# Kernel optimization log

Measured on AMD Instinct MI355X. Metric: run time of the kernel, lower is better.

Reference implementation:

```python
import jax, jax.numpy as jnp
import numpy as np

# raster settings (match init_kwargs)
H, W = 512, 512
TANFOVX, TANFOVY = 0.5, 0.5
DENSITY_SHIFT = -2.0
SCALE_MOD = 1.0
SH_DEG = 2
N, R, D = 262144, 8, 8

SH_C0 = 0.28209479177387814
SH_C1 = 0.4886025119029199
SH_C2 = (1.0925484305920792, -1.0925484305920792, 0.31539156525252005,
         -1.0925484305920792, 0.5462742152960396)


def _camera():
    # row-vector convention: p_view = p_world @ V[:3,:3] + V[3,:3]
    view = np.eye(4, dtype=np.float32)
    view[3, 2] = 3.0  # camera at (0,0,-3) looking down +z
    znear, zfar = 0.01, 100.0
    top, right = TANFOVY * znear, TANFOVX * znear
    P = np.zeros((4, 4), np.float32)
    P[0, 0] = znear / right
    P[1, 1] = znear / top
    P[2, 2] = zfar / (zfar - znear)
    P[2, 3] = 1.0
    P[3, 2] = -zfar * znear / (zfar - znear)
    proj = view @ P  # full world->clip, row-vector convention
    campos = np.array([0.0, 0.0, -3.0], np.float32)
    return jnp.asarray(view), jnp.asarray(proj), jnp.asarray(campos)


def setup_inputs() -> dict:
    key = jax.random.key(0)
    ks = jax.random.split(key, 6)
    positions = jax.random.uniform(ks[0], (N, 3), jnp.float32)          # local coords in [0,1]
    trivecs = jax.random.normal(ks[1], (N, R, 3, D), jnp.float32)
    densities = jax.random.normal(ks[2], (N, R), jnp.float32)
    shs = jax.random.normal(ks[3], (N, R, (SH_DEG + 1) ** 2, 3), jnp.float32) * 0.3
    view, proj, campos = _camera()
    aabb = jnp.array([-1.0, -1.0, -1.0, 2.0, 2.0, 2.0], jnp.float32)    # [origin, size]
    bg = jnp.zeros((3,), jnp.float32)
    rnd = jnp.full((H, W, 3), 0.5, jnp.float32)
    rnd = rnd.at[..., 2].set(jax.random.uniform(ks[4], (H, W), jnp.float32))
    return {"positions": positions, "trivecs": trivecs, "densities": densities,
            "shs": shs, "viewmatrix": view, "projmatrix": proj, "campos": campos,
            "aabb": aabb, "bg": bg, "random_image": rnd}


def _rasterize(positions, trivecs, densities, shs, viewmatrix, projmatrix, campos, aabb, bg):
    world = aabb[:3] + positions * aabb[3:]                              # [N,3]
    ones = jnp.ones((world.shape[0], 1), world.dtype)
    ph = jnp.concatenate([world, ones], 1) @ projmatrix                  # [N,4]
    ndc = ph[:, :3] / (ph[:, 3:4] + 1e-7)
    pview = world @ viewmatrix[:3, :3] + viewmatrix[3, :3]
    depth = pview[:, 2]                                                  # [N]
    ix = jnp.round(((ndc[:, 0] + 1.0) * W - 1.0) * 0.5).astype(jnp.int32)
    iy = jnp.round(((ndc[:, 1] + 1.0) * H - 1.0) * 0.5).astype(jnp.int32)
    valid = (depth > 0.2) & (ix >= 0) & (ix < W) & (iy >= 0) & (iy < H)
    pid = jnp.where(valid, iy * W + ix, H * W)                           # dump bucket H*W

    # trivec density at the cell center: product of the three axis vectors
    mid = trivecs[:, :, :, D // 2]                                       # [N,R,3]
    tri = jax.nn.relu(jnp.prod(mid, axis=-1))                            # [N,R]
    sigma_r = jnp.exp(densities + DENSITY_SHIFT) * tri * SCALE_MOD       # [N,R]
    sigma = sigma_r.sum(-1)
    alpha = jnp.clip(1.0 - jnp.exp(-sigma), 0.0, 0.999)                  # [N]

    # per-rank SH color, density-weighted over ranks
    dirs = world - campos
    dirs = dirs / (jnp.linalg.norm(dirs, axis=-1, keepdims=True) + 1e-8)
    x, y, z = dirs[:, 0:1], dirs[:, 1:2], dirs[:, 2:3]
    basis = jnp.concatenate([
        jnp.full_like(x, SH_C0),
        -SH_C1 * y, SH_C1 * z, -SH_C1 * x,
        SH_C2[0] * x * y, SH_C2[1] * y * z,
        SH_C2[2] * (2.0 * z * z - x * x - y * y),
        SH_C2[3] * x * z, SH_C2[4] * (x * x - y * y)], axis=1)           # [N,9]
    color_r = jnp.maximum(jnp.einsum('nk,nrkc->nrc', basis, shs) + 0.5, 0.0)
    wr = sigma_r / (sigma + 1e-8)[:, None]
    color = jnp.einsum('nr,nrc->nc', wr, color_r)                        # [N,3]

    # depth-sorted per-pixel alpha compositing via segmented exclusive cumsum
    order = jnp.lexsort((depth, pid))
    pid_s, a_s = pid[order], alpha[order]
    c_s, d_s = color[order], depth[order]
    logs = jnp.log1p(-a_s)
    excl = jnp.cumsum(logs) - logs                                       # exclusive cumsum
    first = jnp.searchsorted(pid_s, pid_s, side='left')                  # segment start idx
    T = jnp.exp(excl - excl[first])                                      # transmittance
    wgt = a_s * T
    npx = H * W
    img_c = jax.ops.segment_sum(wgt[:, None] * c_s, pid_s, num_segments=npx + 1)[:npx]
    img_a = jax.ops.segment_sum(wgt, pid_s, num_segments=npx + 1)[:npx]
    img_d = jax.ops.segment_sum(wgt * d_s, pid_s, num_segments=npx + 1)[:npx]
    img_c = img_c + (1.0 - img_a)[:, None] * bg
    pct_d = img_d / (img_a + 1e-8)
    return (img_c.reshape(H, W, 3).transpose(2, 0, 1),
            img_d.reshape(H, W), img_a.reshape(H, W), pct_d.reshape(H, W))


def reference(positions, trivecs, densities, shs, viewmatrix, projmatrix, campos, aabb, bg, random_image):
    # random_image is only used for stochastic jitter in the CUDA kernel; deterministic here
    return _rasterize(positions, trivecs, densities, shs, viewmatrix, projmatrix, campos, aabb, bg)
```

## Files before the change

kernel.cpp:

```cpp
#include <hip/hip_runtime.h>
#include <math.h>
#include <float.h>

#define Hh 512
#define Ww 512
#define HWW (Hh*Ww)
#define NP 262144
#define RR 8


__global__ __launch_bounds__(256) void point_kernel(
    const float* __restrict__ positions,
    const float* __restrict__ trivecs,
    const float* __restrict__ densities,
    const float* __restrict__ shs,
    const float* __restrict__ viewm,
    const float* __restrict__ projm,
    const float* __restrict__ campos,
    const float* __restrict__ aabb,
    float* __restrict__ recs,
    int* __restrict__ counts)
{
#pragma clang fp contract(off)
    int n = blockIdx.x * blockDim.x + threadIdx.x;
    if (n >= NP) return;

    float px = positions[n*3+0], py = positions[n*3+1], pz = positions[n*3+2];
    float wx = aabb[0] + px*aabb[3];
    float wy = aabb[1] + py*aabb[4];
    float wz = aabb[2] + pz*aabb[5];

    float phx = ((wx*projm[0] + wy*projm[4]) + wz*projm[8])  + projm[12];
    float phy = ((wx*projm[1] + wy*projm[5]) + wz*projm[9])  + projm[13];
    float phw = ((wx*projm[3] + wy*projm[7]) + wz*projm[11]) + projm[15];
    float denom = phw + 1e-7f;
    float ndcx = phx / denom;
    float ndcy = phy / denom;
    float depth = ((wx*viewm[2] + wy*viewm[6]) + wz*viewm[10]) + viewm[14];

    float fx = ((ndcx + 1.0f)*(float)Ww - 1.0f)*0.5f;
    float fy = ((ndcy + 1.0f)*(float)Hh - 1.0f)*0.5f;
    int ix = (int)rintf(fx);
    int iy = (int)rintf(fy);
    bool valid = (depth > 0.2f) && (ix >= 0) && (ix < Ww) && (iy >= 0) && (iy < Hh);
    int pid = valid ? (iy*Ww + ix) : -1;

    float4 d0 = *(const float4*)(densities + (size_t)n*RR);
    float4 d1 = *(const float4*)(densities + (size_t)n*RR + 4);
    float den[8] = {d0.x,d0.y,d0.z,d0.w,d1.x,d1.y,d1.z,d1.w};
    const float* tv = trivecs + (size_t)n*RR*24;
    float sr[RR]; float sigma = 0.0f;
    #pragma unroll
    for (int r = 0; r < RR; r++){
        float m0 = tv[r*24 + 4];
        float m1 = tv[r*24 + 12];
        float m2 = tv[r*24 + 20];
        float tri = m0*m1*m2;
        tri = tri > 0.0f ? tri : 0.0f;
        float s = expf(den[r] - 2.0f) * tri;
        sr[r] = s; sigma += s;
    }
    float alpha = 1.0f - expf(-sigma);
    alpha = fminf(alpha, 0.999f);
    alpha = fmaxf(alpha, 0.0f);

    float dxr = wx - campos[0], dyr = wy - campos[1], dzr = wz - campos[2];
    float nrm = sqrtf((dxr*dxr + dyr*dyr) + dzr*dzr) + 1e-8f;
    float x = dxr/nrm, y = dyr/nrm, z = dzr/nrm;
    float basis[9];
    basis[0] = 0.28209479177387814f;
    basis[1] = -0.4886025119029199f * y;
    basis[2] =  0.4886025119029199f * z;
    basis[3] = -0.4886025119029199f * x;
    basis[4] =  1.0925484305920792f * (x*y);
    basis[5] = -1.0925484305920792f * (y*z);
    basis[6] =  0.31539156525252005f * (2.0f*z*z - x*x - y*y);
    basis[7] = -1.0925484305920792f * (x*z);
    basis[8] =  0.5462742152960396f * (x*x - y*y);

    float dot[RR][3];
    #pragma unroll
    for (int r = 0; r < RR; r++){ dot[r][0]=0.f; dot[r][1]=0.f; dot[r][2]=0.f; }
    const float4* sp = (const float4*)(shs + (size_t)n*(RR*27));
    #pragma unroll
    for (int j = 0; j < 54; j++){
        float4 v = sp[j];
        float e[4] = {v.x, v.y, v.z, v.w};
        #pragma unroll
        for (int q = 0; q < 4; q++){
            int f = 4*j + q;
            int r = f / 27;
            int k = (f % 27) / 3;
            int c = f % 3;
            dot[r][c] = fmaf(basis[k], e[q], dot[r][c]);
        }
    }
    float invs = 1.0f/(sigma + 1e-8f);
    float cr = 0.f, cg = 0.f, cb = 0.f;
    #pragma unroll
    for (int r = 0; r < RR; r++){
        float wr = sr[r]*invs;
        cr = fmaf(wr, fmaxf(dot[r][0] + 0.5f, 0.0f), cr);
        cg = fmaf(wr, fmaxf(dot[r][1] + 0.5f, 0.0f), cg);
        cb = fmaf(wr, fmaxf(dot[r][2] + 0.5f, 0.0f), cb);
    }

    float4 ra = make_float4(depth, alpha, cr, cg);
    float4 rb = make_float4(cb, __int_as_float(n), __int_as_float(pid), 0.0f);
    float4* rp = (float4*)(recs + (size_t)n*8);
    rp[0] = ra; rp[1] = rb;
    if (pid >= 0) atomicAdd(&counts[pid], 1);
}

__global__ __launch_bounds__(256) void scan1_kernel(const int* __restrict__ counts,
                                                    int* __restrict__ blockSums)
{
    __shared__ int lds[256];
    int b = blockIdx.x, t = threadIdx.x;
    int4 v = ((const int4*)(counts + (size_t)b*1024))[t];
    int s = v.x + v.y + v.z + v.w;
    lds[t] = s; __syncthreads();
    for (int off = 128; off > 0; off >>= 1){
        if (t < off) lds[t] += lds[t + off];
        __syncthreads();
    }
    if (t == 0) blockSums[b] = lds[0];
}

__global__ __launch_bounds__(256) void scan2_kernel(int* __restrict__ blockSums,
                                                    int* __restrict__ offsets)
{
    __shared__ int lds[256];
    int t = threadIdx.x;
    int v = blockSums[t];
    lds[t] = v; __syncthreads();
    #pragma unroll
    for (int off = 1; off < 256; off <<= 1){
        int add = (t >= off) ? lds[t - off] : 0;
        __syncthreads();
        lds[t] += add;
        __syncthreads();
    }
    blockSums[t] = lds[t] - v;
    if (t == 255) offsets[HWW] = lds[255];
}

__global__ __launch_bounds__(256) void scan3_kernel(const int* __restrict__ counts,
                                                    const int* __restrict__ blockOffs,
                                                    int* __restrict__ offsets,
                                                    int* __restrict__ cursor)
{
    __shared__ int lds[256];
    int b = blockIdx.x, t = threadIdx.x;
    int4 v = ((const int4*)(counts + (size_t)b*1024))[t];
    int s = v.x + v.y + v.z + v.w;
    lds[t] = s; __syncthreads();
    #pragma unroll
    for (int off = 1; off < 256; off <<= 1){
        int add = (t >= off) ? lds[t - off] : 0;
        __syncthreads();
        lds[t] += add;
        __syncthreads();
    }
    int base = blockOffs[b] + (lds[t] - s);
    int4 o;
    o.x = base;
    o.y = o.x + v.x;
    o.z = o.y + v.y;
    o.w = o.z + v.z;
    ((int4*)(offsets + (size_t)b*1024))[t] = o;
    ((int4*)(cursor  + (size_t)b*1024))[t] = o;
}

__global__ __launch_bounds__(256) void scatter_kernel(const float* __restrict__ recs,
                                                      int* __restrict__ cursor,
                                                      float* __restrict__ srecs)
{
    int n = blockIdx.x * blockDim.x + threadIdx.x;
    if (n >= NP) return;
    const float4* rp = (const float4*)(recs + (size_t)n*8);
    float4 ra = rp[0], rb = rp[1];
    int pid = __float_as_int(rb.z);
    if (pid < 0) return;
    int slot = atomicAdd(&cursor[pid], 1);
    float4* sp = (float4*)(srecs + (size_t)slot*8);
    sp[0] = ra; sp[1] = rb;
}

__global__ __launch_bounds__(256) void composite_kernel(const int* __restrict__ offsets,
                                                        const float* __restrict__ srecs,
                                                        const float* __restrict__ bg,
                                                        float* __restrict__ out)
{
    int p = blockIdx.x * blockDim.x + threadIdx.x;
    if (p >= HWW) return;
    int s = offsets[p], e = offsets[p+1];
    float T = 1.0f, accA = 0.f, accD = 0.f, aR = 0.f, aG = 0.f, aB = 0.f;
    float lastD = -FLT_MAX; int lastI = -1;
    for (int it = s; it < e; ++it){
        float bd = FLT_MAX; int bi = 0x7fffffff; int bj = -1;
        for (int j = s; j < e; ++j){
            float4 ra = *(const float4*)(srecs + (size_t)j*8);
            float4 rb = *(const float4*)(srecs + (size_t)j*8 + 4);
            float dj = ra.x; int ij = __float_as_int(rb.y);
            bool gt = (dj > lastD) || (dj == lastD && ij > lastI);
            bool lt = (dj < bd)   || (dj == bd   && ij < bi);
            if (gt && lt){ bd = dj; bi = ij; bj = j; }
        }
        float4 ra = *(const float4*)(srecs + (size_t)bj*8);
        float4 rb = *(const float4*)(srecs + (size_t)bj*8 + 4);
        float a = ra.y;
        float w = a*T;
        aR += w*ra.z; aG += w*ra.w; aB += w*rb.x;
        accA += w; accD += w*ra.x;
        T *= (1.0f - a);
        lastD = bd; lastI = bi;
    }
    float om = 1.0f - accA;
    out[p]         = aR + om*bg[0];
    out[HWW + p]   = aG + om*bg[1];
    out[2*HWW + p] = aB + om*bg[2];
    out[3*HWW + p] = accD;
    out[4*HWW + p] = accA;
    out[5*HWW + p] = accD/(accA + 1e-8f);
}

extern "C" void kernel_launch(void* const* d_in, const int* in_sizes, int n_in,
                              void* d_out, int out_size, void* d_ws, size_t ws_size,
                              hipStream_t stream)
{
    const float* positions = (const float*)d_in[0];
    const float* trivecs   = (const float*)d_in[1];
    const float* densities = (const float*)d_in[2];
    const float* shs       = (const float*)d_in[3];
    const float* viewm     = (const float*)d_in[4];
    const float* projm     = (const float*)d_in[5];
    const float* campos    = (const float*)d_in[6];
    const float* aabb      = (const float*)d_in[7];
    const float* bg        = (const float*)d_in[8];
    float* out = (float*)d_out;

    char* ws = (char*)d_ws;
    size_t o = 0;
    int* counts    = (int*)(ws + o); o += (size_t)HWW*4;
    int* offsets   = (int*)(ws + o); o += ((size_t)HWW + 64)*4;
    int* cursor    = (int*)(ws + o); o += (size_t)HWW*4;
    int* blockSums = (int*)(ws + o); o += 4096;
    float* recs    = (float*)(ws + o); o += (size_t)NP*32;
    float* srecs   = (float*)(ws + o); o += (size_t)NP*32;

    hipMemsetAsync(counts, 0, (size_t)HWW*4, stream);
    point_kernel<<<NP/256, 256, 0, stream>>>(positions, trivecs, densities, shs,
                                             viewm, projm, campos, aabb, recs, counts);
    scan1_kernel<<<HWW/1024, 256, 0, stream>>>(counts, blockSums);
    scan2_kernel<<<1, 256, 0, stream>>>(blockSums, offsets);
    scan3_kernel<<<HWW/1024, 256, 0, stream>>>(counts, blockSums, offsets, cursor);
    scatter_kernel<<<NP/256, 256, 0, stream>>>(recs, cursor, srecs);
    composite_kernel<<<HWW/256, 256, 0, stream>>>(offsets, srecs, bg, out);
}
```

Measured before the change: 551.1 us.

## Replace count/scan/scatter binning with per-pixel linked lists and split point work across lanes

Drops the counting, three-stage scan and scatter kernels. Points now push themselves onto per-pixel linked lists with atomicExch, and the composite kernel walks each list, insertion-sorts up to 32 packed depth/index keys in registers, then blends in order. The O(k^2) selection loop is kept only as a fallback for longer lists. Two threads now share each point, splitting the rank loop and combining sigma and color with lane shuffles. In exchange, the composite stage does dependent pointer-chasing loads, and keys[32] of 64-bit values may spill to scratch.

```diff
diff --git a/kernel.cpp b/kernel.cpp
--- a/kernel.cpp
+++ b/kernel.cpp
@@ -7,6 +7,7 @@
 #define HWW (Hh*Ww)
 #define NP 262144
 #define RR 8
+#define KMAX 32
 
 
 __global__ __launch_bounds__(256) void point_kernel(
@@ -19,11 +20,12 @@
     const float* __restrict__ campos,
     const float* __restrict__ aabb,
     float* __restrict__ recs,
-    int* __restrict__ counts)
+    int* __restrict__ heads)
 {
 #pragma clang fp contract(off)
-    int n = blockIdx.x * blockDim.x + threadIdx.x;
-    if (n >= NP) return;
+    int gid = blockIdx.x * blockDim.x + threadIdx.x;
+    int n    = gid >> 1;
+    int half = gid & 1;
 
     float px = positions[n*3+0], py = positions[n*3+1], pz = positions[n*3+2];
     float wx = aabb[0] + px*aabb[3];
@@ -45,21 +47,21 @@
     bool valid = (depth > 0.2f) && (ix >= 0) && (ix < Ww) && (iy >= 0) && (iy < Hh);
     int pid = valid ? (iy*Ww + ix) : -1;
 
-    float4 d0 = *(const float4*)(densities + (size_t)n*RR);
-    float4 d1 = *(const float4*)(densities + (size_t)n*RR + 4);
-    float den[8] = {d0.x,d0.y,d0.z,d0.w,d1.x,d1.y,d1.z,d1.w};
-    const float* tv = trivecs + (size_t)n*RR*24;
-    float sr[RR]; float sigma = 0.0f;
-    #pragma unroll
-    for (int r = 0; r < RR; r++){
+    float4 d = *(const float4*)(densities + (size_t)n*RR + half*4);
+    float den[4] = {d.x, d.y, d.z, d.w};
+    const float* tv = trivecs + (size_t)n*RR*24 + half*4*24;
+    float sr[4]; float sig_half = 0.0f;
+    #pragma unroll
+    for (int r = 0; r < 4; r++){
         float m0 = tv[r*24 + 4];
         float m1 = tv[r*24 + 12];
         float m2 = tv[r*24 + 20];
         float tri = m0*m1*m2;
         tri = tri > 0.0f ? tri : 0.0f;
         float s = expf(den[r] - 2.0f) * tri;
-        sr[r] = s; sigma += s;
-    }
+        sr[r] = s; sig_half += s;
+    }
+    float sigma = sig_half + __shfl_xor(sig_half, 1, 64);
     float alpha = 1.0f - expf(-sigma);
     alpha = fminf(alpha, 0.999f);
     alpha = fmaxf(alpha, 0.0f);
@@ -78,12 +80,12 @@
     basis[7] = -1.0925484305920792f * (x*z);
     basis[8] =  0.5462742152960396f * (x*x - y*y);
 
-    float dot[RR][3];
-    #pragma unroll
-    for (int r = 0; r < RR; r++){ dot[r][0]=0.f; dot[r][1]=0.f; dot[r][2]=0.f; }
-    const float4* sp = (const float4*)(shs + (size_t)n*(RR*27));
-    #pragma unroll
-    for (int j = 0; j < 54; j++){
+    float dot[4][3];
+    #pragma unroll
+    for (int r = 0; r < 4; r++){ dot[r][0]=0.f; dot[r][1]=0.f; dot[r][2]=0.f; }
+    const float4* sp = (const float4*)(shs + (size_t)n*(RR*27)) + half*27;
+    #pragma unroll
+    for (int j = 0; j < 27; j++){
         float4 v = sp[j];
         float e[4] = {v.x, v.y, v.z, v.w};
         #pragma unroll
@@ -98,124 +100,87 @@
     float invs = 1.0f/(sigma + 1e-8f);
     float cr = 0.f, cg = 0.f, cb = 0.f;
     #pragma unroll
-    for (int r = 0; r < RR; r++){
+    for (int r = 0; r < 4; r++){
         float wr = sr[r]*invs;
         cr = fmaf(wr, fmaxf(dot[r][0] + 0.5f, 0.0f), cr);
         cg = fmaf(wr, fmaxf(dot[r][1] + 0.5f, 0.0f), cg);
         cb = fmaf(wr, fmaxf(dot[r][2] + 0.5f, 0.0f), cb);
     }
-
-    float4 ra = make_float4(depth, alpha, cr, cg);
-    float4 rb = make_float4(cb, __int_as_float(n), __int_as_float(pid), 0.0f);
-    float4* rp = (float4*)(recs + (size_t)n*8);
-    rp[0] = ra; rp[1] = rb;
-    if (pid >= 0) atomicAdd(&counts[pid], 1);
+    cr += __shfl_xor(cr, 1, 64);
+    cg += __shfl_xor(cg, 1, 64);
+    cb += __shfl_xor(cb, 1, 64);
+
+    if (half == 0 && pid >= 0){
+        int next = atomicExch(&heads[pid], n);
+        float4* rp = (float4*)(recs + (size_t)n*8);
+        rp[0] = make_float4(depth, alpha, cr, cg);
+        rp[1] = make_float4(cb, __int_as_float(next), 0.0f, 0.0f);
+    }
 }
 
-__global__ __launch_bounds__(256) void scan1_kernel(const int* __restrict__ counts,
-                                                    int* __restrict__ blockSums)
-{
-    __shared__ int lds[256];
-    int b = blockIdx.x, t = threadIdx.x;
-    int4 v = ((const int4*)(counts + (size_t)b*1024))[t];
-    int s = v.x + v.y + v.z + v.w;
-    lds[t] = s; __syncthreads();
-    for (int off = 128; off > 0; off >>= 1){
-        if (t < off) lds[t] += lds[t + off];
-        __syncthreads();
-    }
-    if (t == 0) blockSums[b] = lds[0];
-}
-
-__global__ __launch_bounds__(256) void scan2_kernel(int* __restrict__ blockSums,
-                                                    int* __restrict__ offsets)
-{
-    __shared__ int lds[256];
-    int t = threadIdx.x;
-    int v = blockSums[t];
-    lds[t] = v; __syncthreads();
-    #pragma unroll
-    for (int off = 1; off < 256; off <<= 1){
-        int add = (t >= off) ? lds[t - off] : 0;
-        __syncthreads();
-        lds[t] += add;
-        __syncthreads();
-    }
-    blockSums[t] = lds[t] - v;
-    if (t == 255) offsets[HWW] = lds[255];
-}
-
-__global__ __launch_bounds__(256) void scan3_kernel(const int* __restrict__ counts,
-                                                    const int* __restrict__ blockOffs,
-                                                    int* __restrict__ offsets,
-                                                    int* __restrict__ cursor)
-{
-    __shared__ int lds[256];
-    int b = blockIdx.x, t = threadIdx.x;
-    int4 v = ((const int4*)(counts + (size_t)b*1024))[t];
-    int s = v.x + v.y + v.z + v.w;
-    lds[t] = s; __syncthreads();
-    #pragma unroll
-    for (int off = 1; off < 256; off <<= 1){
-        int add = (t >= off) ? lds[t - off] : 0;
-        __syncthreads();
-        lds[t] += add;
-        __syncthreads();
-    }
-    int base = blockOffs[b] + (lds[t] - s);
-    int4 o;
-    o.x = base;
-    o.y = o.x + v.x;
-    o.z = o.y + v.y;
-    o.w = o.z + v.z;
-    ((int4*)(offsets + (size_t)b*1024))[t] = o;
-    ((int4*)(cursor  + (size_t)b*1024))[t] = o;
-}
-
-__global__ __launch_bounds__(256) void scatter_kernel(const float* __restrict__ recs,
-                                                      int* __restrict__ cursor,
-                                                      float* __restrict__ srecs)
-{
-    int n = blockIdx.x * blockDim.x + threadIdx.x;
-    if (n >= NP) return;
-    const float4* rp = (const float4*)(recs + (size_t)n*8);
-    float4 ra = rp[0], rb = rp[1];
-    int pid = __float_as_int(rb.z);
-    if (pid < 0) return;
-    int slot = atomicAdd(&cursor[pid], 1);
-    float4* sp = (float4*)(srecs + (size_t)slot*8);
-    sp[0] = ra; sp[1] = rb;
-}
-
-__global__ __launch_bounds__(256) void composite_kernel(const int* __restrict__ offsets,
-                                                        const float* __restrict__ srecs,
-                                                        const float* __restrict__ bg,
-                                                        float* __restrict__ out)
+__global__ __launch_bounds__(256) void composite_kernel(
+    const int* __restrict__ heads,
+    const float* __restrict__ recs,
+    const float* __restrict__ bg,
+    float* __restrict__ out)
 {
     int p = blockIdx.x * blockDim.x + threadIdx.x;
     if (p >= HWW) return;
-    int s = offsets[p], e = offsets[p+1];
+
+    unsigned long long keys[KMAX];
+    int cnt = 0;
+    int cur = heads[p];
+    while (cur >= 0){
+        float dpt = recs[(size_t)cur*8 + 0];
+        int  nxt  = __float_as_int(recs[(size_t)cur*8 + 5]);
+        if (cnt < KMAX)
+            keys[cnt] = ((unsigned long long)__float_as_uint(dpt) << 32) |
+                        (unsigned int)cur;
+        cnt++;
+        cur = nxt;
+    }
+
     float T = 1.0f, accA = 0.f, accD = 0.f, aR = 0.f, aG = 0.f, aB = 0.f;
-    float lastD = -FLT_MAX; int lastI = -1;
-    for (int it = s; it < e; ++it){
-        float bd = FLT_MAX; int bi = 0x7fffffff; int bj = -1;
-        for (int j = s; j < e; ++j){
-            float4 ra = *(const float4*)(srecs + (size_t)j*8);
-            float4 rb = *(const float4*)(srecs + (size_t)j*8 + 4);
-            float dj = ra.x; int ij = __float_as_int(rb.y);
-            bool gt = (dj > lastD) || (dj == lastD && ij > lastI);
-            bool lt = (dj < bd)   || (dj == bd   && ij < bi);
-            if (gt && lt){ bd = dj; bi = ij; bj = j; }
-        }
-        float4 ra = *(const float4*)(srecs + (size_t)bj*8);
-        float4 rb = *(const float4*)(srecs + (size_t)bj*8 + 4);
-        float a = ra.y;
-        float w = a*T;
-        aR += w*ra.z; aG += w*ra.w; aB += w*rb.x;
-        accA += w; accD += w*ra.x;
-        T *= (1.0f - a);
-        lastD = bd; lastI = bi;
-    }
+
+    if (cnt <= KMAX){
+        for (int i = 1; i < cnt; i++){
+            unsigned long long k = keys[i];
+            int j = i - 1;
+            while (j >= 0 && keys[j] > k){ keys[j+1] = keys[j]; j--; }
+            keys[j+1] = k;
+        }
+        for (int i = 0; i < cnt; i++){
+            int nidx = (int)(keys[i] & 0xffffffffu);
+            float4 ra = *(const float4*)(recs + (size_t)nidx*8);
+            float4 rb = *(const float4*)(recs + (size_t)nidx*8 + 4);
+            float a = ra.y, w = a*T;
+            aR += w*ra.z; aG += w*ra.w; aB += w*rb.x;
+            accA += w; accD += w*ra.x;
+            T *= (1.0f - a);
+        }
+    } else {
+        unsigned long long last = 0; bool haveLast = false;
+        for (int it = 0; it < cnt; ++it){
+            unsigned long long best = ~0ull; int bn = -1;
+            for (int c2 = heads[p]; c2 >= 0; ){
+                float dpt = recs[(size_t)c2*8 + 0];
+                int  nxt  = __float_as_int(recs[(size_t)c2*8 + 5]);
+                unsigned long long k =
+                    ((unsigned long long)__float_as_uint(dpt) << 32) |
+                    (unsigned int)c2;
+                if ((!haveLast || k > last) && k < best){ best = k; bn = c2; }
+                c2 = nxt;
+            }
+            float4 ra = *(const float4*)(recs + (size_t)bn*8);
+            float4 rb = *(const float4*)(recs + (size_t)bn*8 + 4);
+            float a = ra.y, w = a*T;
+            aR += w*ra.z; aG += w*ra.w; aB += w*rb.x;
+            accA += w; accD += w*ra.x;
+            T *= (1.0f - a);
+            last = best; haveLast = true;
+        }
+    }
+
     float om = 1.0f - accA;
     out[p]         = aR + om*bg[0];
     out[HWW + p]   = aG + om*bg[1];
@@ -242,19 +207,12 @@
 
     char* ws = (char*)d_ws;
     size_t o = 0;
-    int* counts    = (int*)(ws + o); o += (size_t)HWW*4;
-    int* offsets   = (int*)(ws + o); o += ((size_t)HWW + 64)*4;
-    int* cursor    = (int*)(ws + o); o += (size_t)HWW*4;
-    int* blockSums = (int*)(ws + o); o += 4096;
-    float* recs    = (float*)(ws + o); o += (size_t)NP*32;
-    float* srecs   = (float*)(ws + o); o += (size_t)NP*32;
-
-    hipMemsetAsync(counts, 0, (size_t)HWW*4, stream);
-    point_kernel<<<NP/256, 256, 0, stream>>>(positions, trivecs, densities, shs,
-                                             viewm, projm, campos, aabb, recs, counts);
-    scan1_kernel<<<HWW/1024, 256, 0, stream>>>(counts, blockSums);
-    scan2_kernel<<<1, 256, 0, stream>>>(blockSums, offsets);
-    scan3_kernel<<<HWW/1024, 256, 0, stream>>>(counts, blockSums, offsets, cursor);
-    scatter_kernel<<<NP/256, 256, 0, stream>>>(recs, cursor, srecs);
-    composite_kernel<<<HWW/256, 256, 0, stream>>>(offsets, srecs, bg, out);
+    int*   heads = (int*)(ws + o);   o += (size_t)HWW*4;
+    float* recs  = (float*)(ws + o); o += (size_t)NP*32;
+
+    hipMemsetAsync(heads, 0xFF, (size_t)HWW*4, stream);
+    point_kernel<<<(NP*2)/256, 256, 0, stream>>>(positions, trivecs, densities, shs,
+                                                 viewm, projm, campos, aabb,
+                                                 recs, heads);
+    composite_kernel<<<HWW/256, 256, 0, stream>>>(heads, recs, bg, out);
 }
```

Result: faster. 510.2 us (-7.4%).
